# Optimization experiments

Hardware: AMD Instinct MI355X
Metric: run time of the kernel (lower is better)

## Reference

```python
import jax, jax.numpy as jnp
import numpy as np

B, T, D = 2, 2048, 2048
H, G = 16, 4            # query heads, kv groups
HD = D // H             # head_dim = 128
GS = H // G             # group_size = 4
EPS = 1e-6
ROPE_BASE = 10000.0


def setup_inputs() -> dict:
    key = jax.random.key(0)
    ks = jax.random.split(key, 5)
    s = 0.02
    return {
        "x": jax.random.normal(ks[0], (B, T, D), jnp.float32),
        "Wq": jax.random.normal(ks[1], (H * HD, D), jnp.float32) * s,
        "Wk": jax.random.normal(ks[2], (G * HD, D), jnp.float32) * s,
        "Wv": jax.random.normal(ks[3], (G * HD, D), jnp.float32) * s,
        "Wo": jax.random.normal(ks[4], (D, H * HD), jnp.float32) * s,
        "qn_w": jnp.ones((HD,), jnp.float32),
        "kn_w": jnp.ones((HD,), jnp.float32),
    }


def _rmsnorm(x, w):
    var = jnp.mean(x * x, axis=-1, keepdims=True)
    return x * jax.lax.rsqrt(var + EPS) * w


def _rope_tables(t, d):
    inv_freq = 1.0 / (ROPE_BASE ** (jnp.arange(0, d, 2, dtype=jnp.float32) / d))
    freqs = jnp.arange(t, dtype=jnp.float32)[:, None] * inv_freq[None, :]
    emb = jnp.concatenate([freqs, freqs], axis=-1)  # [T, d]
    return jnp.cos(emb), jnp.sin(emb)


def _apply_rope(x, cos, sin):
    # x: [b, h, t, d]
    d2 = x.shape[-1] // 2
    x1, x2 = x[..., :d2], x[..., d2:]
    rot = jnp.concatenate([-x2, x1], axis=-1)
    return x * cos + rot * sin


def reference(x, Wq, Wk, Wv, Wo, qn_w, kn_w):
    b, t, _ = x.shape
    q = (x @ Wq.T).reshape(b, t, H, HD).transpose(0, 2, 1, 3)  # [b,H,t,hd]
    k = (x @ Wk.T).reshape(b, t, G, HD).transpose(0, 2, 1, 3)  # [b,G,t,hd]
    v = (x @ Wv.T).reshape(b, t, G, HD).transpose(0, 2, 1, 3)

    q = _rmsnorm(q, qn_w)
    k = _rmsnorm(k, kn_w)

    cos, sin = _rope_tables(t, HD)
    q = _apply_rope(q, cos, sin)
    k = _apply_rope(k, cos, sin)

    # torch code scales q by hd^-0.5, then SDPA applies default hd^-0.5 again
    scale = (HD ** -0.5) * (HD ** -0.5)

    # GQA without materializing repeat_interleave: group query heads
    qg = q.reshape(b, G, GS, t, HD)
    scores = jnp.einsum("bgxqd,bgkd->bgxqk", qg, k) * scale  # [b,G,GS,t,t]
    causal = jnp.tril(jnp.ones((t, t), bool))
    scores = jnp.where(causal, scores, -jnp.inf)
    attn = jax.nn.softmax(scores, axis=-1)
    ctx = jnp.einsum("bgxqk,bgkd->bgxqd", attn, v)  # [b,G,GS,t,hd]
    ctx = ctx.reshape(b, H, t, HD).transpose(0, 2, 1, 3).reshape(b, t, H * HD)
    return ctx @ Wo.T
```

## Files before the change

### kernel.cpp

```cpp
#include <hip/hip_runtime.h>
#include <hip/hip_bf16.h>

#define B_ 2
#define T_ 2048
#define D_ 2048
#define H_ 16
#define G_ 4
#define HD_ 128
#define GS_ (H_/G_)

typedef _Float16 half8 __attribute__((ext_vector_type(8)));
typedef _Float16 half2_t __attribute__((ext_vector_type(2)));
typedef float f32x4 __attribute__((ext_vector_type(4)));
typedef float f32x16 __attribute__((ext_vector_type(16)));
typedef int int4_t __attribute__((ext_vector_type(4)));

#define KV_TILE_BYTES 35840
#define KROW_F16 136
#define VROW_F16 72
#define VBASE_F16 8704

#define C0_ 1048576
#define C1_ 1572864
#define C2_ 1703936
#define C3_ 1835008
#define C4_ 2359296
__global__ void cvt_all(const float* __restrict__ sx, const float* __restrict__ sq,
                        const float* __restrict__ sk, const float* __restrict__ sv,
                        const float* __restrict__ so,
                        _Float16* __restrict__ dx, _Float16* __restrict__ dq,
                        _Float16* __restrict__ dk, _Float16* __restrict__ dv,
                        _Float16* __restrict__ dw) {
    int g = blockIdx.x * blockDim.x + threadIdx.x;
    int stride = blockDim.x * gridDim.x;
    for (; g < C4_; g += stride) {
        const float* src; _Float16* dst; int local;
        if (g < C0_)      { src = sx; dst = dx; local = g; }
        else if (g < C1_) { src = sq; dst = dq; local = g - C0_; }
        else if (g < C2_) { src = sk; dst = dk; local = g - C1_; }
        else if (g < C3_) { src = sv; dst = dv; local = g - C2_; }
        else              { src = so; dst = dw; local = g - C3_; }
        f32x4 a = *((const f32x4*)src + local * 2);
        f32x4 b = *((const f32x4*)src + local * 2 + 1);
        half8 hv;
        hv[0] = (_Float16)a[0]; hv[1] = (_Float16)a[1];
        hv[2] = (_Float16)a[2]; hv[3] = (_Float16)a[3];
        hv[4] = (_Float16)b[0]; hv[5] = (_Float16)b[1];
        hv[6] = (_Float16)b[2]; hv[7] = (_Float16)b[3];
        *((half8*)dst + local) = hv;
    }
}

__global__ void rope_tables_k(float* __restrict__ cosT, float* __restrict__ sinT) {
    int i = blockIdx.x * blockDim.x + threadIdx.x;
    int t = i >> 6, l = i & 63;
    float inv_freq = powf(10000.0f, -((float)(2 * l)) / 128.0f);
    float a = (float)t * inv_freq;
    cosT[i] = cosf(a);
    sinT[i] = sinf(a);
}

__global__ void __launch_bounds__(256, 6) gemm_tile64(const _Float16* __restrict__ A,
                                                      const _Float16* __restrict__ B0,
                                                      float* __restrict__ C0, int n0t,
                                                      const _Float16* __restrict__ B1,
                                                      float* __restrict__ C1, int n1t,
                                                      const _Float16* __restrict__ B2,
                                                      float* __restrict__ C2, int n2t,
                                                      int Kd, int nyt) {
    __shared__ _Float16 sA[64 * 32];
    __shared__ _Float16 sB[128 * 32];

    int nwg = gridDim.x;
    int id = blockIdx.x;
    int wg = (id & 7) * (nwg >> 3) + (id >> 3);
    int by = wg % nyt;
    int bx = wg / nyt;

    int tid = threadIdx.x;
    int w = tid >> 6, lane = tid & 63;
    int l15 = lane & 15, g4 = lane >> 4;
    int wm = w & 1, wn = w >> 1;

    const _Float16* Bsel;
    float* Csel;
    int ldc, cb;
    if (by < n0t)            { Bsel = B0; Csel = C0; ldc = n0t * 128; cb = by; }
    else if (by < n0t + n1t) { Bsel = B1; Csel = C1; ldc = n1t * 128; cb = by - n0t; }
    else                     { Bsel = B2; Csel = C2; ldc = n2t * 128; cb = by - n0t - n1t; }

    const _Float16* Ab = A + (size_t)(bx * 64) * Kd;
    const _Float16* Bb = Bsel + (size_t)(cb * 128) * Kd;

    int sb1 = tid + 256;
    size_t gaA  = (size_t)(tid >> 2) * Kd + (tid & 3) * 8;
    size_t gaB1 = (size_t)(sb1 >> 2) * Kd + (sb1 & 3) * 8;
    _Float16* dA  = sA + (size_t)tid * 8;
    _Float16* dB0 = sB + (size_t)tid * 8;
    _Float16* dB1 = sB + (size_t)sb1 * 8;

    #define STAGE(K0)                                                                      \
        do {                                                                               \
            __builtin_amdgcn_global_load_lds(                                              \
                (const __attribute__((address_space(1))) unsigned int*)(Ab + gaA + (K0)),  \
                (__attribute__((address_space(3))) unsigned int*)dA, 16, 0, 0);            \
            __builtin_amdgcn_global_load_lds(                                              \
                (const __attribute__((address_space(1))) unsigned int*)(Bb + gaA + (K0)),  \
                (__attribute__((address_space(3))) unsigned int*)dB0, 16, 0, 0);           \
            __builtin_amdgcn_global_load_lds(                                              \
                (const __attribute__((address_space(1))) unsigned int*)(Bb + gaB1 + (K0)), \
                (__attribute__((address_space(3))) unsigned int*)dB1, 16, 0, 0);           \
        } while (0)

    f32x4 acc[2][4];
    #pragma unroll
    for (int i = 0; i < 2; i++)
        #pragma unroll
        for (int j = 0; j < 4; j++) acc[i][j] = (f32x4){0.f, 0.f, 0.f, 0.f};

    STAGE(0);

    int nIt = Kd >> 5;
    for (int it = 0; it < nIt; ++it) {
        __syncthreads();

        half8 af[2], bf[4];
        #pragma unroll
        for (int mi = 0; mi < 2; mi++)
            af[mi] = *(const half8*)&sA[(wm * 32 + mi * 16 + l15) * 32 + g4 * 8];
        #pragma unroll
        for (int ni = 0; ni < 4; ni++)
            bf[ni] = *(const half8*)&sB[(wn * 64 + ni * 16 + l15) * 32 + g4 * 8];

        #pragma unroll
        for (int mi = 0; mi < 2; mi++)
            #pragma unroll
            for (int ni = 0; ni < 4; ni++)
                acc[mi][ni] = __builtin_amdgcn_mfma_f32_16x16x32_f16(af[mi], bf[ni], acc[mi][ni], 0, 0, 0);

        if (it + 1 < nIt) {
            __syncthreads();
            STAGE((size_t)(it + 1) * 32);
        }
    }
    #undef STAGE

    int rbase = bx * 64 + wm * 32 + g4 * 4;
    int cbase = cb * 128 + wn * 64 + l15;
    #pragma unroll
    for (int mi = 0; mi < 2; mi++)
        #pragma unroll
        for (int r = 0; r < 4; r++) {
            float* crow = Csel + (size_t)(rbase + mi * 16 + r) * ldc + cbase;
            #pragma unroll
            for (int ni = 0; ni < 4; ni++) crow[ni * 16] = acc[mi][ni][r];
        }
}

__global__ void rmsnorm_rope_qk(float* __restrict__ Qf, float* __restrict__ Kf,
                                const float* __restrict__ qw, const float* __restrict__ kw,
                                const float* __restrict__ cosT, const float* __restrict__ sinT,
                                _Float16* __restrict__ qH) {
    int gw = (int)((blockIdx.x * (size_t)blockDim.x + threadIdx.x) >> 6);
    int lane = threadIdx.x & 63;
    bool isQ = gw < (B_ * T_ * H_);
    int row_i = isQ ? gw : gw - (B_ * T_ * H_);
    int heads = isQ ? H_ : G_;
    const float* wv = isQ ? qw : kw;
    float* row = (isQ ? Qf : Kf) + (size_t)row_i * HD_;
    int t = (row_i / heads) % T_;
    float x0 = row[lane];
    float x1 = row[lane + 64];
    float ss = x0 * x0 + x1 * x1;
    #pragma unroll
    for (int off = 1; off < 64; off <<= 1) ss += __shfl_xor(ss, off);
    float inv = rsqrtf(ss * (1.0f / 128.0f) + 1e-6f);
    float n0 = x0 * inv * wv[lane];
    float n1 = x1 * inv * wv[lane + 64];
    float c = cosT[t * 64 + lane];
    float s = sinT[t * 64 + lane];
    float r0 = n0 * c - n1 * s;
    float r1 = n1 * c + n0 * s;
    if (isQ) {
        qH[(size_t)row_i * HD_ + lane]      = (_Float16)(r0 * (1.0f / 128.0f));
        qH[(size_t)row_i * HD_ + lane + 64] = (_Float16)(r1 * (1.0f / 128.0f));
    } else {
        row[lane]      = r0;
        row[lane + 64] = r1;
    }
}

__global__ void __launch_bounds__(256) pack_kv(const float* __restrict__ kf,
                                               const float* __restrict__ vf,
                                               _Float16* __restrict__ img) {
    int bid = blockIdx.x;
    int tile = bid & 31, g = (bid >> 5) & 3, b = bid >> 7;
    int tid = threadIdx.x;
    _Float16* out = img + (size_t)bid * (KV_TILE_BYTES / 2);

    #pragma unroll
    for (int it = 0; it < 5; it++) {
        int gi = tid + 256 * it;
        if (gi < 64 * 17) {
            int key = gi / 17, gr = gi % 17;
            half8 hv = (half8){0, 0, 0, 0, 0, 0, 0, 0};
            if (gr < 16) {
                const float* src = kf + ((size_t)((b * T_ + tile * 64 + key) * G_ + g)) * HD_ + gr * 8;
                #pragma unroll
                for (int j = 0; j < 8; j++) hv[j] = (_Float16)src[j];
            }
            *(half8*)(out + (size_t)gi * 8) = hv;
        }
    }
    #pragma unroll
    for (int it = 0; it < 5; it++) {
        int vi = tid + 256 * it;
        if (vi < 128 * 9) {
            int d = vi / 9, gr = vi % 9;
            half8 hv = (half8){0, 0, 0, 0, 0, 0, 0, 0};
            if (gr < 8) {
                const float* src = vf + ((size_t)((b * T_ + tile * 64 + gr * 8) * G_ + g)) * HD_ + d;
                #pragma unroll
                for (int j = 0; j < 8; j++) hv[j] = (_Float16)src[(size_t)j * (G_ * HD_)];
            }
            *(half8*)(out + VBASE_F16 + (size_t)vi * 8) = hv;
        }
    }
}

__global__ void __launch_bounds__(256, 2) attn_mfma4(const _Float16* __restrict__ qh,
                                                     const _Float16* __restrict__ kvimg,
                                                     _Float16* __restrict__ ctx) {
    int id = blockIdx.x;
    int hlf = id >> 8, rr0 = id & 255;
    int qb = hlf ? (15 - (rr0 & 15)) : (rr0 & 15);
    int hb = (rr0 >> 4) | (hlf << 4);
    int h = hb & 15, b = hb >> 4;
    int g = h >> 2;

    int tid = threadIdx.x;
    int w = tid >> 6, lane = tid & 63;
    int l31 = lane & 31, hi = lane >> 5;

    __shared__ __align__(16) char sKV[2][KV_TILE_BYTES];

    int qW = qb * 128 + w * 32;
    int qme = qW + l31;

    half8 qfrag[8];
    {
        const _Float16* qrow = qh + ((size_t)(b * T_ + qme)) * (H_ * HD_) + h * HD_ + hi * 8;
        #pragma unroll
        for (int ks = 0; ks < 8; ks++) qfrag[ks] = *(const half8*)(qrow + ks * 16);
    }

    f32x16 o[4];
    #pragma unroll
    for (int dt2 = 0; dt2 < 4; dt2++)
        #pragma unroll
        for (int r = 0; r < 16; r++) o[dt2][r] = 0.f;
    float m = -INFINITY, lsum = 0.f;

    const char* ibase = (const char*)kvimg + (size_t)((b * 4 + g) * 32) * KV_TILE_BYTES;

    #define STAGE_T(BUF, KT)                                                                       \
        do {                                                                                       \
            const char* src_ = ibase + (size_t)(KT) * KV_TILE_BYTES;                               \
            char* dst_ = &sKV[BUF][0];                                                             \
            _Pragma("unroll")                                                                      \
            for (int i_ = 0; i_ < 9; i_++) {                                                       \
                int c_ = w + 4 * i_;                                                               \
                if (c_ < 35) {                                                                     \
                    __builtin_amdgcn_global_load_lds(                                              \
                        (const __attribute__((address_space(1))) unsigned int*)(src_ + c_ * 1024 + lane * 16), \
                        (__attribute__((address_space(3))) unsigned int*)(dst_ + c_ * 1024 + lane * 16), 16, 0, 0); \
                }                                                                                  \
            }                                                                                      \
        } while (0)

    int nt = 2 * qb + 2;
    int ktmax_w = (qW + 31) >> 6;

    STAGE_T(0, 0);
    int cur = 0;

    for (int kt = 0; kt < nt; kt++) {
        __syncthreads();
        if (kt + 1 < nt) STAGE_T(cur ^ 1, kt + 1);

        if (kt <= ktmax_w) {
            const char* bufK = &sKV[cur][0];
            const char* bufV = &sKV[cur][0] + VBASE_F16 * 2;

            f32x16 stc[2];
            #pragma unroll
            for (int kt2 = 0; kt2 < 2; kt2++)
                #pragma unroll
                for (int r = 0; r < 16; r++) stc[kt2][r] = 0.f;

            __builtin_amdgcn_s_setprio(1);
            #pragma unroll
            for (int ks = 0; ks < 8; ks++) {
                #pragma unroll
                for (int kt2 = 0; kt2 < 2; kt2++) {
                    half8 kfr = *(const half8*)(bufK + (kt2 * 32 + l31) * (KROW_F16 * 2) + ks * 32 + hi * 16);
                    stc[kt2] = __builtin_amdgcn_mfma_f32_32x32x16_f16(kfr, qfrag[ks], stc[kt2], 0, 0, 0);
                }
            }
            __builtin_amdgcn_s_setprio(0);

            #pragma unroll
            for (int kt2 = 0; kt2 < 2; kt2++)
                #pragma unroll
                for (int reg = 0; reg < 16; reg++) {
                    int key = kt * 64 + kt2 * 32 + 8 * (reg >> 2) + 4 * hi + (reg & 3);
                    float v = stc[kt2][reg];
                    stc[kt2][reg] = (key <= qme) ? v : -INFINITY;
                }

            float pmax = -INFINITY;
            #pragma unroll
            for (int kt2 = 0; kt2 < 2; kt2++)
                #pragma unroll
                for (int reg = 0; reg < 16; reg++) pmax = fmaxf(pmax, stc[kt2][reg]);
            pmax = fmaxf(pmax, __shfl_xor(pmax, 32));

            if (__any(!(pmax - m <= 8.0f))) {
                float nm = fmaxf(m, pmax);
                float alpha = __expf(m - nm);
                lsum *= alpha;
                #pragma unroll
                for (int reg = 0; reg < 16; reg++) {
                    float ar = __shfl(alpha, 8 * (reg >> 2) + 4 * hi + (reg & 3));
                    #pragma unroll
                    for (int dt2 = 0; dt2 < 4; dt2++) o[dt2][reg] *= ar;
                }
                m = nm;
            }

            float rsum = 0.f;
            #pragma unroll
            for (int kt2 = 0; kt2 < 2; kt2++)
                #pragma unroll
                for (int reg = 0; reg < 16; reg++) {
                    float e = __expf(stc[kt2][reg] - m);
                    stc[kt2][reg] = e;
                    rsum += e;
                }
            rsum += __shfl_xor(rsum, 32);
            lsum += rsum;

            int pk[16];
            #pragma unroll
            for (int kt2 = 0; kt2 < 2; kt2++)
                #pragma unroll
                for (int oo = 0; oo < 4; oo++)
                    #pragma unroll
                    for (int c = 0; c < 2; c++) {
                        half2_t hp;
                        hp[0] = (_Float16)stc[kt2][4 * oo + 2 * c];
                        hp[1] = (_Float16)stc[kt2][4 * oo + 2 * c + 1];
                        pk[kt2 * 8 + 2 * oo + c] = __builtin_bit_cast(int, hp);
                    }

            __builtin_amdgcn_s_setprio(1);
            #pragma unroll
            for (int ks = 0; ks < 4; ks++) {
                int base = (ks >> 1) * 8 + (ks & 1) * 4;
                int z0 = hi ? pk[base + 0] : pk[base + 2];
                int z1 = hi ? pk[base + 1] : pk[base + 3];
                int xz0 = __shfl_xor(z0, 32);
                int xz1 = __shfl_xor(z1, 32);
                int4_t pi;
                pi[0] = hi ? xz0 : pk[base + 0];
                pi[1] = hi ? xz1 : pk[base + 1];
                pi[2] = hi ? pk[base + 2] : xz0;
                pi[3] = hi ? pk[base + 3] : xz1;
                half8 pfrag = __builtin_bit_cast(half8, pi);
                #pragma unroll
                for (int dt2 = 0; dt2 < 4; dt2++) {
                    half8 vfr = *(const half8*)(bufV + (dt2 * 32 + l31) * (VROW_F16 * 2) + ks * 32 + hi * 16);
                    o[dt2] = __builtin_amdgcn_mfma_f32_32x32x16_f16(pfrag, vfr, o[dt2], 0, 0, 0);
                }
            }
            __builtin_amdgcn_s_setprio(0);
        }
        cur ^= 1;
    }
    #undef STAGE_T

    float invl = 1.0f / lsum;
    #pragma unroll
    for (int reg = 0; reg < 16; reg++) {
        int qrow = 8 * (reg >> 2) + 4 * hi + (reg & 3);
        float ir = __shfl(invl, qrow);
        _Float16* orow = ctx + (size_t)(b * T_ + qW + qrow) * (H_ * HD_) + h * HD_ + l31;
        #pragma unroll
        for (int dt2 = 0; dt2 < 4; dt2++)
            orow[dt2 * 32] = (_Float16)(o[dt2][reg] * ir);
    }
}

extern "C" void kernel_launch(void* const* d_in, const int* in_sizes, int n_in,
                              void* d_out, int out_size, void* d_ws, size_t ws_size,
                              hipStream_t stream) {
    const float* x   = (const float*)d_in[0];
    const float* Wq  = (const float*)d_in[1];
    const float* Wk  = (const float*)d_in[2];
    const float* Wv  = (const float*)d_in[3];
    const float* Wo  = (const float*)d_in[4];
    const float* qnw = (const float*)d_in[5];
    const float* knw = (const float*)d_in[6];
    float* out = (float*)d_out;

    char* ws = (char*)d_ws;
    size_t off = 0;
    auto alloc = [&](size_t bytes) {
        char* p = ws + off;
        off += (bytes + 255) & ~(size_t)255;
        return p;
    };
    _Float16* x_h  = (_Float16*)alloc((size_t)B_ * T_ * D_ * 2);
    _Float16* wq_h = (_Float16*)alloc((size_t)H_ * HD_ * D_ * 2);
    _Float16* wk_h = (_Float16*)alloc((size_t)G_ * HD_ * D_ * 2);
    _Float16* wv_h = (_Float16*)alloc((size_t)G_ * HD_ * D_ * 2);
    _Float16* wo_h = (_Float16*)alloc((size_t)D_ * H_ * HD_ * 2);
    float* q_f = (float*)alloc((size_t)B_ * T_ * H_ * HD_ * 4);
    float* k_f = (float*)alloc((size_t)B_ * T_ * G_ * HD_ * 4);
    float* v_f = (float*)alloc((size_t)B_ * T_ * G_ * HD_ * 4);
    _Float16* ctx_h = (_Float16*)alloc((size_t)B_ * T_ * H_ * HD_ * 2);
    float* cosT = (float*)alloc((size_t)T_ * 64 * 4);
    float* sinT = (float*)alloc((size_t)T_ * 64 * 4);

    _Float16* q_h   = x_h;
    _Float16* kvimg = wq_h;

    cvt_all<<<2048, 256, 0, stream>>>(x, Wq, Wk, Wv, Wo, x_h, wq_h, wk_h, wv_h, wo_h);
    rope_tables_k<<<(T_ * 64) / 256, 256, 0, stream>>>(cosT, sinT);

    gemm_tile64<<<64 * 24, 256, 0, stream>>>(x_h, wq_h, q_f, 16,
                                             wk_h, k_f, 4,
                                             wv_h, v_f, 4, D_, 24);

    rmsnorm_rope_qk<<<(B_ * T_ * (H_ + G_)) / 4, 256, 0, stream>>>(q_f, k_f, qnw, knw, cosT, sinT, q_h);

    pack_kv<<<256, 256, 0, stream>>>(k_f, v_f, kvimg);

    attn_mfma4<<<512, 256, 0, stream>>>(q_h, kvimg, ctx_h);

    gemm_tile64<<<64 * 16, 256, 0, stream>>>(ctx_h, wo_h, out, 16,
                                             nullptr, nullptr, 0,
                                             nullptr, nullptr, 0, H_ * HD_, 16);
}
```

Measured before the change: 253.3 us.

## Enlarge GEMM tile to 128x128 with double-buffered async LDS loads

```diff
diff --git a/kernel.cpp b/kernel.cpp
--- a/kernel.cpp
+++ b/kernel.cpp
@@ -60,95 +60,102 @@
     sinT[i] = sinf(a);
 }
 
-__global__ void __launch_bounds__(256, 6) gemm_tile64(const _Float16* __restrict__ A,
-                                                      const _Float16* __restrict__ B0,
-                                                      float* __restrict__ C0, int n0t,
-                                                      const _Float16* __restrict__ B1,
-                                                      float* __restrict__ C1, int n1t,
-                                                      const _Float16* __restrict__ B2,
-                                                      float* __restrict__ C2, int n2t,
-                                                      int Kd, int nyt) {
-    __shared__ _Float16 sA[64 * 32];
-    __shared__ _Float16 sB[128 * 32];
-
-    int nwg = gridDim.x;
-    int id = blockIdx.x;
-    int wg = (id & 7) * (nwg >> 3) + (id >> 3);
-    int by = wg % nyt;
-    int bx = wg / nyt;
+__global__ void __launch_bounds__(256) gemm_tile(const _Float16* __restrict__ A,
+                                                 const _Float16* __restrict__ B0,
+                                                 float* __restrict__ C0, int n0t,
+                                                 const _Float16* __restrict__ B1,
+                                                 float* __restrict__ C1, int n1t,
+                                                 const _Float16* __restrict__ B2,
+                                                 float* __restrict__ C2, int n2t,
+                                                 int Kd) {
+    __shared__ _Float16 sA[2][128 * 32];
+    __shared__ _Float16 sB[2][128 * 32];
 
     int tid = threadIdx.x;
     int w = tid >> 6, lane = tid & 63;
     int l15 = lane & 15, g4 = lane >> 4;
-    int wm = w & 1, wn = w >> 1;
-
+    int wm = w >> 1, wn = w & 1;
+
+    int y = blockIdx.y;
     const _Float16* Bsel;
     float* Csel;
     int ldc, cb;
-    if (by < n0t)            { Bsel = B0; Csel = C0; ldc = n0t * 128; cb = by; }
-    else if (by < n0t + n1t) { Bsel = B1; Csel = C1; ldc = n1t * 128; cb = by - n0t; }
-    else                     { Bsel = B2; Csel = C2; ldc = n2t * 128; cb = by - n0t - n1t; }
-
-    const _Float16* Ab = A + (size_t)(bx * 64) * Kd;
+    if (y < n0t)            { Bsel = B0; Csel = C0; ldc = n0t * 128; cb = y; }
+    else if (y < n0t + n1t) { Bsel = B1; Csel = C1; ldc = n1t * 128; cb = y - n0t; }
+    else                    { Bsel = B2; Csel = C2; ldc = n2t * 128; cb = y - n0t - n1t; }
+
+    const _Float16* Ab = A + (size_t)(blockIdx.x * 128) * Kd;
     const _Float16* Bb = Bsel + (size_t)(cb * 128) * Kd;
 
-    int sb1 = tid + 256;
-    size_t gaA  = (size_t)(tid >> 2) * Kd + (tid & 3) * 8;
-    size_t gaB1 = (size_t)(sb1 >> 2) * Kd + (sb1 & 3) * 8;
-    _Float16* dA  = sA + (size_t)tid * 8;
-    _Float16* dB0 = sB + (size_t)tid * 8;
-    _Float16* dB1 = sB + (size_t)sb1 * 8;
-
-    #define STAGE(K0)                                                                      \
-        do {                                                                               \
-            __builtin_amdgcn_global_load_lds(                                              \
-                (const __attribute__((address_space(1))) unsigned int*)(Ab + gaA + (K0)),  \
-                (__attribute__((address_space(3))) unsigned int*)dA, 16, 0, 0);            \
-            __builtin_amdgcn_global_load_lds(                                              \
-                (const __attribute__((address_space(1))) unsigned int*)(Bb + gaA + (K0)),  \
-                (__attribute__((address_space(3))) unsigned int*)dB0, 16, 0, 0);           \
-            __builtin_amdgcn_global_load_lds(                                              \
-                (const __attribute__((address_space(1))) unsigned int*)(Bb + gaB1 + (K0)), \
-                (__attribute__((address_space(3))) unsigned int*)dB1, 16, 0, 0);           \
+    int s0 = w * 128 + lane;
+    int s1 = s0 + 64;
+    size_t ga0 = (size_t)(s0 >> 2) * Kd + (s0 & 3) * 8;
+    size_t ga1 = (size_t)(s1 >> 2) * Kd + (s1 & 3) * 8;
+
+    #define STAGE(BUF, K0)                                                                     \
+        do {                                                                                   \
+            _Float16* a0_ = &sA[BUF][0] + (size_t)(w * 2) * 512;                               \
+            _Float16* a1_ = &sA[BUF][0] + (size_t)(w * 2 + 1) * 512;                           \
+            _Float16* b0_ = &sB[BUF][0] + (size_t)(w * 2) * 512;                               \
+            _Float16* b1_ = &sB[BUF][0] + (size_t)(w * 2 + 1) * 512;                           \
+            __builtin_amdgcn_global_load_lds(                                                  \
+                (const __attribute__((address_space(1))) unsigned int*)(Ab + ga0 + (K0)),      \
+                (__attribute__((address_space(3))) unsigned int*)a0_, 16, 0, 0);               \
+            __builtin_amdgcn_global_load_lds(                                                  \
+                (const __attribute__((address_space(1))) unsigned int*)(Ab + ga1 + (K0)),      \
+                (__attribute__((address_space(3))) unsigned int*)a1_, 16, 0, 0);               \
+            __builtin_amdgcn_global_load_lds(                                                  \
+                (const __attribute__((address_space(1))) unsigned int*)(Bb + ga0 + (K0)),      \
+                (__attribute__((address_space(3))) unsigned int*)b0_, 16, 0, 0);               \
+            __builtin_amdgcn_global_load_lds(                                                  \
+                (const __attribute__((address_space(1))) unsigned int*)(Bb + ga1 + (K0)),      \
+                (__attribute__((address_space(3))) unsigned int*)b1_, 16, 0, 0);               \
         } while (0)
 
-    f32x4 acc[2][4];
-    #pragma unroll
-    for (int i = 0; i < 2; i++)
+    f32x4 acc[4][4];
+    #pragma unroll
+    for (int i = 0; i < 4; i++)
         #pragma unroll
         for (int j = 0; j < 4; j++) acc[i][j] = (f32x4){0.f, 0.f, 0.f, 0.f};
 
-    STAGE(0);
-
     int nIt = Kd >> 5;
+    STAGE(0, 0);
+    if (nIt > 1) STAGE(1, 32);
+
     for (int it = 0; it < nIt; ++it) {
-        __syncthreads();
-
-        half8 af[2], bf[4];
-        #pragma unroll
-        for (int mi = 0; mi < 2; mi++)
-            af[mi] = *(const half8*)&sA[(wm * 32 + mi * 16 + l15) * 32 + g4 * 8];
+        int cur = it & 1;
+        if (it + 1 < nIt) asm volatile("s_waitcnt vmcnt(4)" ::: "memory");
+        else              asm volatile("s_waitcnt vmcnt(0)" ::: "memory");
+        __builtin_amdgcn_sched_barrier(0);
+        __builtin_amdgcn_s_barrier();
+        __builtin_amdgcn_sched_barrier(0);
+
+        half8 af[4], bf[4];
+        #pragma unroll
+        for (int mi = 0; mi < 4; mi++)
+            af[mi] = *(const half8*)&sA[cur][(wm * 64 + mi * 16 + l15) * 32 + g4 * 8];
         #pragma unroll
         for (int ni = 0; ni < 4; ni++)
-            bf[ni] = *(const half8*)&sB[(wn * 64 + ni * 16 + l15) * 32 + g4 * 8];
-
-        #pragma unroll
-        for (int mi = 0; mi < 2; mi++)
+            bf[ni] = *(const half8*)&sB[cur][(wn * 64 + ni * 16 + l15) * 32 + g4 * 8];
+
+        #pragma unroll
+        for (int mi = 0; mi < 4; mi++)
             #pragma unroll
             for (int ni = 0; ni < 4; ni++)
                 acc[mi][ni] = __builtin_amdgcn_mfma_f32_16x16x32_f16(af[mi], bf[ni], acc[mi][ni], 0, 0, 0);
 
-        if (it + 1 < nIt) {
-            __syncthreads();
-            STAGE((size_t)(it + 1) * 32);
-        }
+        __builtin_amdgcn_sched_barrier(0);
+        asm volatile("" ::: "memory");
+        __builtin_amdgcn_s_barrier();
+        __builtin_amdgcn_sched_barrier(0);
+        if (it + 2 < nIt) STAGE(cur, (size_t)(it + 2) * 32);
     }
     #undef STAGE
 
-    int rbase = bx * 64 + wm * 32 + g4 * 4;
+    int rbase = blockIdx.x * 128 + wm * 64 + g4 * 4;
     int cbase = cb * 128 + wn * 64 + l15;
     #pragma unroll
-    for (int mi = 0; mi < 2; mi++)
+    for (int mi = 0; mi < 4; mi++)
         #pragma unroll
         for (int r = 0; r < 4; r++) {
             float* crow = Csel + (size_t)(rbase + mi * 16 + r) * ldc + cbase;
@@ -438,9 +445,9 @@
     cvt_all<<<2048, 256, 0, stream>>>(x, Wq, Wk, Wv, Wo, x_h, wq_h, wk_h, wv_h, wo_h);
     rope_tables_k<<<(T_ * 64) / 256, 256, 0, stream>>>(cosT, sinT);
 
-    gemm_tile64<<<64 * 24, 256, 0, stream>>>(x_h, wq_h, q_f, 16,
-                                             wk_h, k_f, 4,
-                                             wv_h, v_f, 4, D_, 24);
+    gemm_tile<<<dim3(32, 24), 256, 0, stream>>>(x_h, wq_h, q_f, 16,
+                                                wk_h, k_f, 4,
+                                                wv_h, v_f, 4, D_);
 
     rmsnorm_rope_qk<<<(B_ * T_ * (H_ + G_)) / 4, 256, 0, stream>>>(q_f, k_f, qnw, knw, cosT, sinT, q_h);
 
@@ -448,7 +455,7 @@
 
     attn_mfma4<<<512, 256, 0, stream>>>(q_h, kvimg, ctx_h);
 
-    gemm_tile64<<<64 * 16, 256, 0, stream>>>(ctx_h, wo_h, out, 16,
-                                             nullptr, nullptr, 0,
-                                             nullptr, nullptr, 0, H_ * HD_, 16);
-}
+    gemm_tile<<<dim3(32, 16), 256, 0, stream>>>(ctx_h, wo_h, out, 16,
+                                                nullptr, nullptr, 0,
+                                                nullptr, nullptr, 0, H_ * HD_);
+}
```

Result: faster. 218.5 us (-13.7%).
